# Kernel tuning notes

Hardware: AMD Instinct MI355X
Metric: run time of the kernel (lower is better)

The kernel has to match this reference:

```python
import jax, jax.numpy as jnp
import numpy as np

GRID = 256      # spatial grid (periodic, pseudo-spectral)
BATCH = 8
N_STEPS = 4     # dynamics steps between outputs (layer arg N)
N_OUTPUT = 4    # number of outputs (layer arg n_output)
CH = 32         # Q_network hidden channels
DT = 0.01       # timestep
R_DRAG = 0.05   # linear (Ekman) drag
BETA = 0.5      # beta-plane coefficient
Q_SCALE = 0.01  # Q_callback scaling of network output
IN_W = 1.0      # input_weight
OUT_W = 1.0     # output_weight


def _wavenumbers():
    k = jnp.fft.fftfreq(GRID, 1.0 / GRID).astype(jnp.float32)  # integer wavenumbers
    KX = k[None, :]   # x varies along axis 1
    KY = k[:, None]   # y varies along axis 0
    K2 = KX * KX + KY * KY
    inv_lap = jnp.where(K2 > 0, -1.0 / jnp.where(K2 > 0, K2, 1.0), 0.0)  # psi_hat = -zeta_hat/k^2
    return KX, KY, inv_lap


def _q_network(z, W1, b1, W2, b2):
    # 2-layer 3x3 CNN forcing network on a single [H, W] field.
    x = z[None, :, :, None]  # NHWC
    dn = ('NHWC', 'HWIO', 'NHWC')
    h = jax.lax.conv_general_dilated(x, W1, (1, 1), 'SAME', dimension_numbers=dn) + b1
    h = jax.nn.relu(h)
    q = jax.lax.conv_general_dilated(h, W2, (1, 1), 'SAME', dimension_numbers=dn) + b2
    return q[0, :, :, 0]


def setup_inputs() -> dict:
    key = jax.random.key(0)
    k0, k1, k2, k3 = jax.random.split(key, 4)
    zeta = jax.random.normal(k0, (BATCH, GRID, GRID), dtype=jnp.float32)
    Q_0 = 0.1 * jax.random.normal(k1, (GRID, GRID), dtype=jnp.float32)
    W1 = 0.1 * jax.random.normal(k2, (3, 3, 1, CH), dtype=jnp.float32)
    b1 = jnp.zeros((CH,), dtype=jnp.float32)
    W2 = 0.1 * jax.random.normal(k3, (3, 3, CH, 1), dtype=jnp.float32)
    b2 = jnp.zeros((1,), dtype=jnp.float32)
    return {"zeta": zeta, "Q_0": Q_0, "W1": W1, "b1": b1, "W2": W2, "b2": b2}


def reference(zeta, Q_0, W1, b1, W2, b2):
    KX, KY, inv_lap = _wavenumbers()

    @jax.checkpoint
    def step(_, z):
        # Q_0 + Q_callback(dynamics, Q_network), evaluated before each step
        Q = Q_0 + Q_SCALE * _q_network(z, W1, b1, W2, b2)
        zh = jnp.fft.fft2(z)
        ph = zh * inv_lap                                  # solve nabla^2 psi = zeta
        u = jnp.real(jnp.fft.ifft2(-1j * KY * ph))         # u = -dpsi/dy
        v = jnp.real(jnp.fft.ifft2(1j * KX * ph))          # v =  dpsi/dx
        zx = jnp.real(jnp.fft.ifft2(1j * KX * zh))
        zy = jnp.real(jnp.fft.ifft2(1j * KY * zh))
        adv = u * zx + v * zy
        return z + DT * (-adv - BETA * v - R_DRAG * z + Q)

    def compute_step_outputs(z, _):
        z = jax.lax.fori_loop(0, N_STEPS, step, z)
        return z, z * OUT_W

    def compute_outputs(z0):
        _, outs = jax.lax.scan(compute_step_outputs, z0 * IN_W, None, length=N_OUTPUT)
        return outs  # [n_output, H, W]

    return jax.vmap(compute_outputs)(zeta)  # [batch, n_output, H, W]
```

## Files before the change

kernel.cpp:

```cpp
#include <hip/hip_runtime.h>

#define NG 256
#define PI2F 6.28318530717958647692f
#define PIDX(i) ((i) + ((i) >> 4))

__device__ __forceinline__ float2 f2add(float2 a, float2 b){ return make_float2(a.x+b.x, a.y+b.y); }
__device__ __forceinline__ float2 f2sub(float2 a, float2 b){ return make_float2(a.x-b.x, a.y-b.y); }
__device__ __forceinline__ float2 cmul(float2 a, float2 b){ return make_float2(a.x*b.x - a.y*b.y, a.x*b.y + a.y*b.x); }
__device__ __forceinline__ float comp(float4 v, int p) {
    return p == 0 ? v.x : p == 1 ? v.y : p == 2 ? v.z : v.w;
}
__device__ __forceinline__ float4 f4fma(float4 a, float4 v, float s) {
    return make_float4(fmaf(v.x, s, a.x), fmaf(v.y, s, a.y),
                       fmaf(v.z, s, a.z), fmaf(v.w, s, a.w));
}
__device__ __forceinline__ float dot4(float4 a, float4 b) {
    return a.x * b.x + a.y * b.y + a.z * b.z + a.w * b.w;
}

template<bool INV>
__device__ __forceinline__ void fft256_r4(float2* a, float2* b, const float2* tw,
                                          int u, bool act)
{
#pragma unroll
    for (int st = 0; st < 4; ++st) {
        if (act) {
            const int sl = 2 * st;
            const int q  = u & ((1 << sl) - 1);
            const int j1 = u - q;
            const float2 x0 = a[PIDX(u)];
            const float2 x1 = a[PIDX(u + 64)];
            const float2 x2 = a[PIDX(u + 128)];
            const float2 x3 = a[PIDX(u + 192)];
            float2 w1 = tw[j1];
            if (INV) w1.y = -w1.y;
            const float2 w2 = cmul(w1, w1);
            const float2 w3 = cmul(w1, w2);
            const float2 apc = f2add(x0, x2), amc = f2sub(x0, x2);
            const float2 bpd = f2add(x1, x3), bmd = f2sub(x1, x3);
            const float2 jb  = make_float2(-bmd.y, bmd.x);
            const float2 t0  = f2add(apc, bpd);
            const float2 t2  = f2sub(apc, bpd);
            const float2 t1  = INV ? f2add(amc, jb) : f2sub(amc, jb);
            const float2 t3  = INV ? f2sub(amc, jb) : f2add(amc, jb);
            const int wb = q + (j1 << 2);
            const int ss = 1 << sl;
            b[PIDX(wb)]          = t0;
            b[PIDX(wb + ss)]     = cmul(w1, t1);
            b[PIDX(wb + 2 * ss)] = cmul(w2, t2);
            b[PIDX(wb + 3 * ss)] = cmul(w3, t3);
        }
        __syncthreads();
        float2* tmp = a; a = b; b = tmp;
    }
}

__device__ __forceinline__ void init_tw(float2* tw, int tid)
{
    if (tid < 256) {
        float s, c;
        __sincosf(-PI2F * (float)tid * (1.f / 256.f), &s, &c);
        tw[tid] = make_float2(c, s);
    }
}

#define R_POOL 19456

__global__ void __launch_bounds__(256)
r_kernel(const float* zin, float* zout,
         const float2* __restrict__ Ct0, const float2* __restrict__ Ct1,
         float2* __restrict__ At, const float* __restrict__ Qb,
         float* __restrict__ outp, int do_d, int do_a)
{
    __shared__ __align__(16) char pool[R_POOL];
    float2* tw   = (float2*)pool;
    float2* bufs = (float2*)(pool + 2048);
    const int tid = threadIdx.x;
    const int b   = blockIdx.x & 7;
    const int y0  = (blockIdx.x >> 3) * 2;
    const int j   = tid >> 6, u = tid & 63;

    init_tw(tw, tid);

    if (do_d) {
        float2* A = bufs + j * 272;
        float2* B = bufs + (4 + j) * 272;
        const float2* src = ((j & 1) ? Ct1 : Ct0)
                          + ((size_t)(b * NG + y0 + (j >> 1))) * NG;
#pragma unroll
        for (int r4 = 0; r4 < 4; ++r4) {
            const int x = u + 64 * r4;
            A[PIDX(x)] = src[x];
        }
        __syncthreads();
        fft256_r4<true>(A, B, tw, u, true);

        const float sc = 1.f / 256.f;
        float zn01[2];
#pragma unroll
        for (int r = 0; r < 2; ++r) {
            const float2 uvv = (bufs + (2 * r) * 272)[PIDX(tid)];
            const float2 gzz = (bufs + (2 * r + 1) * 272)[PIDX(tid)];
            const float uu = uvv.x * sc, vv = uvv.y * sc;
            const float zx = gzz.x * sc, zy = gzz.y * sc;
            const int idx = (b * NG + y0 + r) * NG + tid;
            const float z0v = zin[idx];
            const float qv  = Qb[idx];
            const float adv = uu * zx + vv * zy;
            const float zn = z0v + 0.01f * (-adv - 0.5f * vv - 0.05f * z0v + qv);
            zout[idx] = zn;
            if (outp) outp[b * (4 * NG * NG) + (y0 + r) * NG + tid] = zn;
            zn01[r] = zn;
        }
        __syncthreads();
        bufs[PIDX(tid)] = make_float2(zn01[0], zn01[1]);
        __syncthreads();
    } else {
        bufs[PIDX(tid)] = make_float2(zin[(b * NG + y0) * NG + tid],
                                      zin[(b * NG + y0 + 1) * NG + tid]);
        __syncthreads();
    }

    if (do_a) {
        fft256_r4<false>(bufs, bufs + 4 * 272, tw, u, j == 0);
        const int k  = tid;
        const int km = (256 - k) & 255;
        const float2 Zk = bufs[PIDX(k)], Zm = bufs[PIDX(km)];
        const float dx = Zk.x - Zm.x, dy = Zk.y + Zm.y;
        const float4 ov = make_float4(0.5f * (Zk.x + Zm.x), 0.5f * (Zk.y - Zm.y),
                                      0.5f * dy, -0.5f * dx);
        *((float4*)(At + ((size_t)(b * NG + k)) * NG + y0)) = ov;
    }
}

#define COL_POOL 51344

__global__ void __launch_bounds__(512)
col_kernel(const float2* __restrict__ At, float2* __restrict__ Ct0,
           float2* __restrict__ Ct1, const float* __restrict__ zsrc,
           const float* __restrict__ Q0, const float* __restrict__ W1,
           const float* __restrict__ b1, const float* __restrict__ W2,
           const float* __restrict__ b2, float* __restrict__ Qb)
{
    __shared__ __align__(16) char pool[COL_POOL];
    const int tid = threadIdx.x;

    if (blockIdx.x >= 512) {
        float*  zt  = (float*)pool;
        float*  ht  = (float*)(pool + 2240);
        float4* w1s = (float4*)(pool + 48896);
        float4* w2s = (float4*)(pool + 50048);
        float*  b1s = (float*)(pool + 51200);
        float*  b2s = (float*)(pool + 51328);
        const int cb  = blockIdx.x - 512;
        const int b   = cb & 7;
        const int tile = cb >> 3;
        const int ty0 = (tile >> 4) * 16, tx0 = (tile & 15) * 16;

        if (tid < 72) {
            w1s[tid] = ((const float4*)W1)[tid];
            w2s[tid] = ((const float4*)W2)[tid];
        }
        if (tid < 32) b1s[tid] = b1[tid];
        if (tid == 0) b2s[0] = b2[0];

        for (int i = tid; i < 120; i += 512) {
            const int r = i / 6, c4 = i - r * 6;
            const int gy = ty0 - 2 + r;
            const int gx = tx0 - 4 + 4 * c4;
            float4 v = make_float4(0.f, 0.f, 0.f, 0.f);
            if ((unsigned)gy < 256u && (unsigned)gx < 256u)
                v = *((const float4*)&zsrc[(b * NG + gy) * NG + gx]);
            *((float4*)&zt[r * 28 + 4 * c4]) = v;
        }
        __syncthreads();

        if (tid < 360) {
            const int chunk = tid >> 2, cgp = tid & 3;
            const int hy = chunk / 5, hx0 = (chunk - hy * 5) * 4;
            const int k4 = hx0;
            float4 hacc[8];
#pragma unroll
            for (int c = 0; c < 8; ++c) {
                const float bv = b1s[cgp * 8 + c];
                hacc[c] = make_float4(bv, bv, bv, bv);
            }
#pragma unroll
            for (int dy = 0; dy < 3; ++dy) {
                const float* zrow = &zt[(hy + dy) * 28 + k4];
                const float4 Az = *((const float4*)zrow);
                const float4 Bz = *((const float4*)(zrow + 4));
                const float4 W0 = make_float4(Az.z, Az.w, Bz.x, Bz.y);
                const float4 W1v = make_float4(Az.w, Bz.x, Bz.y, Bz.z);
#pragma unroll
                for (int g = 0; g < 2; ++g) {
                    const float4 wa = w1s[(dy * 3 + 0) * 8 + 2 * cgp + g];
                    const float4 wb = w1s[(dy * 3 + 1) * 8 + 2 * cgp + g];
                    const float4 wc = w1s[(dy * 3 + 2) * 8 + 2 * cgp + g];
                    hacc[4*g+0] = f4fma(f4fma(f4fma(hacc[4*g+0], W0, wa.x), W1v, wb.x), Bz, wc.x);
                    hacc[4*g+1] = f4fma(f4fma(f4fma(hacc[4*g+1], W0, wa.y), W1v, wb.y), Bz, wc.y);
                    hacc[4*g+2] = f4fma(f4fma(f4fma(hacc[4*g+2], W0, wa.z), W1v, wb.z), Bz, wc.z);
                    hacc[4*g+3] = f4fma(f4fma(f4fma(hacc[4*g+3], W0, wa.w), W1v, wb.w), Bz, wc.w);
                }
            }
            const int gyh = ty0 - 1 + hy;
            const bool vy = (unsigned)gyh < 256u;
#pragma unroll
            for (int p = 0; p < 4; ++p) {
                const int hxc = hx0 + p;
                if (hxc < 18) {
                    const float mk = (vy && (unsigned)(tx0 - 1 + hxc) < 256u) ? 1.f : 0.f;
                    float* cellp = &ht[(hy * 18 + hxc) * 36];
                    const int s0 = ((2 * cgp + 0 + hxc) & 7) << 2;
                    const int s1 = ((2 * cgp + 1 + hxc) & 7) << 2;
                    const float4 lo = make_float4(
                        mk * fmaxf(comp(hacc[0], p), 0.f), mk * fmaxf(comp(hacc[1], p), 0.f),
                        mk * fmaxf(comp(hacc[2], p), 0.f), mk * fmaxf(comp(hacc[3], p), 0.f));
                    const float4 hi = make_float4(
                        mk * fmaxf(comp(hacc[4], p), 0.f), mk * fmaxf(comp(hacc[5], p), 0.f),
                        mk * fmaxf(comp(hacc[6], p), 0.f), mk * fmaxf(comp(hacc[7], p), 0.f));
                    *((float4*)(cellp + s0)) = lo;
                    *((float4*)(cellp + s1)) = hi;
                }
            }
        }
        __syncthreads();

        {
            const int chunk = tid >> 3, cg = tid & 7;
            const int oy = chunk >> 2, ox4 = (chunk & 3) * 4;
            float q0 = 0.f, q1 = 0.f, q2 = 0.f, q3 = 0.f;
#pragma unroll
            for (int dy = 0; dy < 3; ++dy) {
                const float* hrow = &ht[((oy + dy) * 18 + ox4) * 36];
                const float4 wA = w2s[(dy * 3 + 0) * 8 + cg];
                const float4 wB = w2s[(dy * 3 + 1) * 8 + cg];
                const float4 wC = w2s[(dy * 3 + 2) * 8 + cg];
#pragma unroll
                for (int jj = 0; jj < 6; ++jj) {
                    const float4 hv = *((const float4*)(hrow + jj * 36
                                        + (((cg + ox4 + jj) & 7) << 2)));
                    if (jj <= 3) {
                        const float d = dot4(hv, wA);
                        if (jj == 0) q0 += d; else if (jj == 1) q1 += d;
                        else if (jj == 2) q2 += d; else q3 += d;
                    }
                    if (jj >= 1 && jj <= 4) {
                        const float d = dot4(hv, wB);
                        if (jj == 1) q0 += d; else if (jj == 2) q1 += d;
                        else if (jj == 3) q2 += d; else q3 += d;
                    }
                    if (jj >= 2) {
                        const float d = dot4(hv, wC);
                        if (jj == 2) q0 += d; else if (jj == 3) q1 += d;
                        else if (jj == 4) q2 += d; else q3 += d;
                    }
                }
            }
#pragma unroll
            for (int s = 1; s < 8; s <<= 1) {
                q0 += __shfl_xor(q0, s); q1 += __shfl_xor(q1, s);
                q2 += __shfl_xor(q2, s); q3 += __shfl_xor(q3, s);
            }
            if (cg == 0) {
                const int gy = ty0 + oy, gx = tx0 + ox4;
                const float4 Qv = *((const float4*)&Q0[gy * NG + gx]);
                const float bb = b2s[0];
                const float4 o = make_float4(
                    Qv.x + 0.01f * (q0 + bb), Qv.y + 0.01f * (q1 + bb),
                    Qv.z + 0.01f * (q2 + bb), Qv.w + 0.01f * (q3 + bb));
                *((float4*)&Qb[(b * NG + gy) * NG + gx]) = o;
            }
        }
    } else {
        float2* tw   = (float2*)pool;
        float2* bufs = (float2*)(pool + 2048);
        const int bid = blockIdx.x;
        const int b  = bid & 7;
        const int kg = bid >> 3;
        const int j8 = tid >> 6, u = tid & 63;

        init_tw(tw, tid);
        if (j8 < 4) {
            const int kxl = 4 * kg + j8;
            float2* A = bufs + j8 * 272;
            const float2* src = At + ((size_t)(b * NG + kxl)) * NG;
#pragma unroll
            for (int r = 0; r < 4; ++r) {
                const int x = u + 64 * r;
                A[PIDX(x)] = src[x];
            }
        }
        __syncthreads();
        fft256_r4<false>(bufs + j8 * 272, bufs + (4 + (j8 & 3)) * 272, tw, u, j8 < 4);

        if (tid < 256) {
            const int jl = tid >> 6;
            const int kxl = 4 * kg + jl;
            float2* A = bufs + jl * 272;
            float2* C = bufs + (8 + jl) * 272;
            const float kxv = (kxl < 128) ? (float)kxl : (float)(kxl - 256);
            const float kxm = (kxl == 128) ? 0.f : kxv;
#pragma unroll
            for (int r = 0; r < 4; ++r) {
                const int ky = u + 64 * r;
                const float kyv = (ky < 128) ? (float)ky : (float)(ky - 256);
                const float kym = (ky == 128) ? 0.f : kyv;
                const float K2 = kxv * kxv + kyv * kyv;
                const float il = (K2 > 0.f) ? (-1.f / K2) : 0.f;
                const float2 Z = A[PIDX(ky)];
                const float ar = -kxm * il, ai = -kym * il;
                A[PIDX(ky)] = make_float2(ar * Z.x - ai * Z.y, ar * Z.y + ai * Z.x);
                C[PIDX(ky)] = make_float2(-kym * Z.x - kxm * Z.y, -kym * Z.y + kxm * Z.x);
            }
        }
        __syncthreads();

        float2* ia = (j8 < 4) ? bufs + j8 * 272 : bufs + (8 + (j8 - 4)) * 272;
        float2* ib = (j8 < 4) ? bufs + (4 + j8) * 272 : bufs + (12 + (j8 - 4)) * 272;
        fft256_r4<true>(ia, ib, tw, u, true);

        const float sc = 1.f / 256.f;
        const int y = tid & 255;
        float2 ov[4];
        if (tid < 256) {
#pragma unroll
            for (int jj = 0; jj < 4; ++jj) {
                const float2 r0 = (bufs + jj * 272)[PIDX(y)];
                ov[jj] = make_float2(r0.x * sc, r0.y * sc);
            }
            float4* dst = (float4*)(Ct0 + ((size_t)(b * NG + y)) * NG + 4 * kg);
            dst[0] = ((float4*)ov)[0];
            dst[1] = ((float4*)ov)[1];
        } else {
#pragma unroll
            for (int jj = 0; jj < 4; ++jj) {
                const float2 r1 = (bufs + (8 + jj) * 272)[PIDX(y)];
                ov[jj] = make_float2(r1.x * sc, r1.y * sc);
            }
            float4* dst = (float4*)(Ct1 + ((size_t)(b * NG + y)) * NG + 4 * kg);
            dst[0] = ((float4*)ov)[0];
            dst[1] = ((float4*)ov)[1];
        }
    }
}

extern "C" void kernel_launch(void* const* d_in, const int* in_sizes, int n_in,
                              void* d_out, int out_size, void* d_ws, size_t ws_size,
                              hipStream_t stream)
{
    const float* zeta = (const float*)d_in[0];
    const float* Q0   = (const float*)d_in[1];
    const float* W1   = (const float*)d_in[2];
    const float* b1   = (const float*)d_in[3];
    const float* W2   = (const float*)d_in[4];
    const float* b2   = (const float*)d_in[5];
    float* outp = (float*)d_out;

    char* ws = (char*)d_ws;
    float*  zws = (float*)(ws);
    float*  Qb  = (float*)(ws + (2u << 20));
    float2* At  = (float2*)(ws + (4u << 20));
    float2* Ct0 = (float2*)(ws + (8u << 20));
    float2* Ct1 = (float2*)(ws + (12u << 20));
    if (ws_size < (16u << 20)) return;

    r_kernel<<<1024, 256, 0, stream>>>(zeta, zws, Ct0, Ct1, At, Qb,
                                       nullptr, 0, 1);
    for (int j = 1; j <= 16; ++j) {
        const float* zp = (j == 1) ? zeta : zws;
        col_kernel<<<2560, 512, 0, stream>>>(At, Ct0, Ct1, zp,
                                             Q0, W1, b1, W2, b2, Qb);
        float* op = (j % 4 == 0) ? (outp + (size_t)(j / 4 - 1) * NG * NG)
                                 : nullptr;
        r_kernel<<<1024, 256, 0, stream>>>(zp, zws, Ct0, Ct1, At, Qb,
                                           op, 1, (j < 16) ? 1 : 0);
    }
}
```

Measured before the change: 551.9 us.

## Double per-block work in row FFT and CNN kernels to halve block counts

The row kernel now processes four rows per 512-thread block instead of two per 256-thread block, running two independent inverse and forward FFT groups. The CNN part of the column kernel now covers a 16x32 tile per block by looping over two 16x16 subtiles and sharing one halo load and one weight load. The aim is fewer blocks and less repeated twiddle, weight and halo setup. The cost is more shared memory per block, extra barriers inside the CNN loop, and a serialized two-pass CNN that may reduce latency hiding.

```diff
diff --git a/kernel.cpp b/kernel.cpp
--- a/kernel.cpp
+++ b/kernel.cpp
@@ -64,9 +64,9 @@
     }
 }
 
-#define R_POOL 19456
-
-__global__ void __launch_bounds__(256)
+#define R_POOL 36864
+
+__global__ void __launch_bounds__(512)
 r_kernel(const float* zin, float* zout,
          const float2* __restrict__ Ct0, const float2* __restrict__ Ct1,
          float2* __restrict__ At, const float* __restrict__ Qb,
@@ -77,14 +77,15 @@
     float2* bufs = (float2*)(pool + 2048);
     const int tid = threadIdx.x;
     const int b   = blockIdx.x & 7;
-    const int y0  = (blockIdx.x >> 3) * 2;
+    const int y0  = (blockIdx.x >> 3) * 4;
     const int j   = tid >> 6, u = tid & 63;
+    const int col = tid & 255, rp = tid >> 8;
 
     init_tw(tw, tid);
 
     if (do_d) {
         float2* A = bufs + j * 272;
-        float2* B = bufs + (4 + j) * 272;
+        float2* B = bufs + (8 + j) * 272;
         const float2* src = ((j & 1) ? Ct1 : Ct0)
                           + ((size_t)(b * NG + y0 + (j >> 1))) * NG;
 #pragma unroll
@@ -99,41 +100,46 @@
         float zn01[2];
 #pragma unroll
         for (int r = 0; r < 2; ++r) {
-            const float2 uvv = (bufs + (2 * r) * 272)[PIDX(tid)];
-            const float2 gzz = (bufs + (2 * r + 1) * 272)[PIDX(tid)];
+            const int rr = 2 * rp + r;
+            const float2 uvv = (bufs + (2 * rr) * 272)[PIDX(col)];
+            const float2 gzz = (bufs + (2 * rr + 1) * 272)[PIDX(col)];
             const float uu = uvv.x * sc, vv = uvv.y * sc;
             const float zx = gzz.x * sc, zy = gzz.y * sc;
-            const int idx = (b * NG + y0 + r) * NG + tid;
+            const int idx = (b * NG + y0 + rr) * NG + col;
             const float z0v = zin[idx];
             const float qv  = Qb[idx];
             const float adv = uu * zx + vv * zy;
             const float zn = z0v + 0.01f * (-adv - 0.5f * vv - 0.05f * z0v + qv);
             zout[idx] = zn;
-            if (outp) outp[b * (4 * NG * NG) + (y0 + r) * NG + tid] = zn;
+            if (outp) outp[b * (4 * NG * NG) + (y0 + rr) * NG + col] = zn;
             zn01[r] = zn;
         }
         __syncthreads();
-        bufs[PIDX(tid)] = make_float2(zn01[0], zn01[1]);
+        (bufs + 2 * rp * 272)[PIDX(col)] = make_float2(zn01[0], zn01[1]);
         __syncthreads();
     } else {
-        bufs[PIDX(tid)] = make_float2(zin[(b * NG + y0) * NG + tid],
-                                      zin[(b * NG + y0 + 1) * NG + tid]);
+        (bufs + 2 * rp * 272)[PIDX(col)] =
+            make_float2(zin[(b * NG + y0 + 2 * rp) * NG + col],
+                        zin[(b * NG + y0 + 2 * rp + 1) * NG + col]);
         __syncthreads();
     }
 
     if (do_a) {
-        fft256_r4<false>(bufs, bufs + 4 * 272, tw, u, j == 0);
-        const int k  = tid;
+        const int jj = (j < 2) ? j : 1;
+        fft256_r4<false>(bufs + 2 * jj * 272, bufs + (8 + 2 * jj) * 272,
+                         tw, u, j < 2);
+        const int k  = col;
         const int km = (256 - k) & 255;
-        const float2 Zk = bufs[PIDX(k)], Zm = bufs[PIDX(km)];
+        const float2* Aj = bufs + 2 * rp * 272;
+        const float2 Zk = Aj[PIDX(k)], Zm = Aj[PIDX(km)];
         const float dx = Zk.x - Zm.x, dy = Zk.y + Zm.y;
         const float4 ov = make_float4(0.5f * (Zk.x + Zm.x), 0.5f * (Zk.y - Zm.y),
                                       0.5f * dy, -0.5f * dx);
-        *((float4*)(At + ((size_t)(b * NG + k)) * NG + y0)) = ov;
-    }
-}
-
-#define COL_POOL 51344
+        *((float4*)(At + ((size_t)(b * NG + k)) * NG + y0 + 2 * rp)) = ov;
+    }
+}
+
+#define COL_POOL 52624
 
 __global__ void __launch_bounds__(512)
 col_kernel(const float2* __restrict__ At, float2* __restrict__ Ct0,
@@ -147,15 +153,16 @@
 
     if (blockIdx.x >= 512) {
         float*  zt  = (float*)pool;
-        float*  ht  = (float*)(pool + 2240);
-        float4* w1s = (float4*)(pool + 48896);
-        float4* w2s = (float4*)(pool + 50048);
-        float*  b1s = (float*)(pool + 51200);
-        float*  b2s = (float*)(pool + 51328);
+        float*  ht  = (float*)(pool + 3520);
+        float4* w1s = (float4*)(pool + 50176);
+        float4* w2s = (float4*)(pool + 51328);
+        float*  b1s = (float*)(pool + 52480);
+        float*  b2s = (float*)(pool + 52608);
         const int cb  = blockIdx.x - 512;
         const int b   = cb & 7;
-        const int tile = cb >> 3;
-        const int ty0 = (tile >> 4) * 16, tx0 = (tile & 15) * 16;
+        const int pr  = cb >> 3;
+        const int ty0 = (pr >> 3) * 16;
+        const int tx0 = (pr & 7) * 32;
 
         if (tid < 72) {
             w1s[tid] = ((const float4*)W1)[tid];
@@ -164,113 +171,117 @@
         if (tid < 32) b1s[tid] = b1[tid];
         if (tid == 0) b2s[0] = b2[0];
 
-        for (int i = tid; i < 120; i += 512) {
-            const int r = i / 6, c4 = i - r * 6;
+        for (int i = tid; i < 200; i += 512) {
+            const int r = i / 10, c4 = i - r * 10;
             const int gy = ty0 - 2 + r;
             const int gx = tx0 - 4 + 4 * c4;
             float4 v = make_float4(0.f, 0.f, 0.f, 0.f);
             if ((unsigned)gy < 256u && (unsigned)gx < 256u)
                 v = *((const float4*)&zsrc[(b * NG + gy) * NG + gx]);
-            *((float4*)&zt[r * 28 + 4 * c4]) = v;
-        }
-        __syncthreads();
-
-        if (tid < 360) {
-            const int chunk = tid >> 2, cgp = tid & 3;
-            const int hy = chunk / 5, hx0 = (chunk - hy * 5) * 4;
-            const int k4 = hx0;
-            float4 hacc[8];
-#pragma unroll
-            for (int c = 0; c < 8; ++c) {
-                const float bv = b1s[cgp * 8 + c];
-                hacc[c] = make_float4(bv, bv, bv, bv);
-            }
-#pragma unroll
-            for (int dy = 0; dy < 3; ++dy) {
-                const float* zrow = &zt[(hy + dy) * 28 + k4];
-                const float4 Az = *((const float4*)zrow);
-                const float4 Bz = *((const float4*)(zrow + 4));
-                const float4 W0 = make_float4(Az.z, Az.w, Bz.x, Bz.y);
-                const float4 W1v = make_float4(Az.w, Bz.x, Bz.y, Bz.z);
-#pragma unroll
-                for (int g = 0; g < 2; ++g) {
-                    const float4 wa = w1s[(dy * 3 + 0) * 8 + 2 * cgp + g];
-                    const float4 wb = w1s[(dy * 3 + 1) * 8 + 2 * cgp + g];
-                    const float4 wc = w1s[(dy * 3 + 2) * 8 + 2 * cgp + g];
-                    hacc[4*g+0] = f4fma(f4fma(f4fma(hacc[4*g+0], W0, wa.x), W1v, wb.x), Bz, wc.x);
-                    hacc[4*g+1] = f4fma(f4fma(f4fma(hacc[4*g+1], W0, wa.y), W1v, wb.y), Bz, wc.y);
-                    hacc[4*g+2] = f4fma(f4fma(f4fma(hacc[4*g+2], W0, wa.z), W1v, wb.z), Bz, wc.z);
-                    hacc[4*g+3] = f4fma(f4fma(f4fma(hacc[4*g+3], W0, wa.w), W1v, wb.w), Bz, wc.w);
-                }
-            }
-            const int gyh = ty0 - 1 + hy;
-            const bool vy = (unsigned)gyh < 256u;
-#pragma unroll
-            for (int p = 0; p < 4; ++p) {
-                const int hxc = hx0 + p;
-                if (hxc < 18) {
-                    const float mk = (vy && (unsigned)(tx0 - 1 + hxc) < 256u) ? 1.f : 0.f;
-                    float* cellp = &ht[(hy * 18 + hxc) * 36];
-                    const int s0 = ((2 * cgp + 0 + hxc) & 7) << 2;
-                    const int s1 = ((2 * cgp + 1 + hxc) & 7) << 2;
-                    const float4 lo = make_float4(
-                        mk * fmaxf(comp(hacc[0], p), 0.f), mk * fmaxf(comp(hacc[1], p), 0.f),
-                        mk * fmaxf(comp(hacc[2], p), 0.f), mk * fmaxf(comp(hacc[3], p), 0.f));
-                    const float4 hi = make_float4(
-                        mk * fmaxf(comp(hacc[4], p), 0.f), mk * fmaxf(comp(hacc[5], p), 0.f),
-                        mk * fmaxf(comp(hacc[6], p), 0.f), mk * fmaxf(comp(hacc[7], p), 0.f));
-                    *((float4*)(cellp + s0)) = lo;
-                    *((float4*)(cellp + s1)) = hi;
-                }
-            }
-        }
-        __syncthreads();
-
-        {
-            const int chunk = tid >> 3, cg = tid & 7;
-            const int oy = chunk >> 2, ox4 = (chunk & 3) * 4;
-            float q0 = 0.f, q1 = 0.f, q2 = 0.f, q3 = 0.f;
-#pragma unroll
-            for (int dy = 0; dy < 3; ++dy) {
-                const float* hrow = &ht[((oy + dy) * 18 + ox4) * 36];
-                const float4 wA = w2s[(dy * 3 + 0) * 8 + cg];
-                const float4 wB = w2s[(dy * 3 + 1) * 8 + cg];
-                const float4 wC = w2s[(dy * 3 + 2) * 8 + cg];
-#pragma unroll
-                for (int jj = 0; jj < 6; ++jj) {
-                    const float4 hv = *((const float4*)(hrow + jj * 36
-                                        + (((cg + ox4 + jj) & 7) << 2)));
-                    if (jj <= 3) {
-                        const float d = dot4(hv, wA);
-                        if (jj == 0) q0 += d; else if (jj == 1) q1 += d;
-                        else if (jj == 2) q2 += d; else q3 += d;
+            *((float4*)&zt[r * 44 + 4 * c4]) = v;
+        }
+        __syncthreads();
+
+        for (int t = 0; t < 2; ++t) {
+            const int txt = tx0 + 16 * t;
+            if (tid < 360) {
+                const int chunk = tid >> 2, cgp = tid & 3;
+                const int hy = chunk / 5, hx0 = (chunk - hy * 5) * 4;
+                const int k4 = 16 * t + hx0;
+                float4 hacc[8];
+#pragma unroll
+                for (int c = 0; c < 8; ++c) {
+                    const float bv = b1s[cgp * 8 + c];
+                    hacc[c] = make_float4(bv, bv, bv, bv);
+                }
+#pragma unroll
+                for (int dy = 0; dy < 3; ++dy) {
+                    const float* zrow = &zt[(hy + dy) * 44 + k4];
+                    const float4 Az = *((const float4*)zrow);
+                    const float4 Bz = *((const float4*)(zrow + 4));
+                    const float4 W0 = make_float4(Az.z, Az.w, Bz.x, Bz.y);
+                    const float4 W1v = make_float4(Az.w, Bz.x, Bz.y, Bz.z);
+#pragma unroll
+                    for (int g = 0; g < 2; ++g) {
+                        const float4 wa = w1s[(dy * 3 + 0) * 8 + 2 * cgp + g];
+                        const float4 wb = w1s[(dy * 3 + 1) * 8 + 2 * cgp + g];
+                        const float4 wc = w1s[(dy * 3 + 2) * 8 + 2 * cgp + g];
+                        hacc[4*g+0] = f4fma(f4fma(f4fma(hacc[4*g+0], W0, wa.x), W1v, wb.x), Bz, wc.x);
+                        hacc[4*g+1] = f4fma(f4fma(f4fma(hacc[4*g+1], W0, wa.y), W1v, wb.y), Bz, wc.y);
+                        hacc[4*g+2] = f4fma(f4fma(f4fma(hacc[4*g+2], W0, wa.z), W1v, wb.z), Bz, wc.z);
+                        hacc[4*g+3] = f4fma(f4fma(f4fma(hacc[4*g+3], W0, wa.w), W1v, wb.w), Bz, wc.w);
                     }
-                    if (jj >= 1 && jj <= 4) {
-                        const float d = dot4(hv, wB);
-                        if (jj == 1) q0 += d; else if (jj == 2) q1 += d;
-                        else if (jj == 3) q2 += d; else q3 += d;
+                }
+                const int gyh = ty0 - 1 + hy;
+                const bool vy = (unsigned)gyh < 256u;
+#pragma unroll
+                for (int p = 0; p < 4; ++p) {
+                    const int hxc = hx0 + p;
+                    if (hxc < 18) {
+                        const float mk = (vy && (unsigned)(txt - 1 + hxc) < 256u) ? 1.f : 0.f;
+                        float* cellp = &ht[(hy * 18 + hxc) * 36];
+                        const int s0 = ((2 * cgp + 0 + hxc) & 7) << 2;
+                        const int s1 = ((2 * cgp + 1 + hxc) & 7) << 2;
+                        const float4 lo = make_float4(
+                            mk * fmaxf(comp(hacc[0], p), 0.f), mk * fmaxf(comp(hacc[1], p), 0.f),
+                            mk * fmaxf(comp(hacc[2], p), 0.f), mk * fmaxf(comp(hacc[3], p), 0.f));
+                        const float4 hi = make_float4(
+                            mk * fmaxf(comp(hacc[4], p), 0.f), mk * fmaxf(comp(hacc[5], p), 0.f),
+                            mk * fmaxf(comp(hacc[6], p), 0.f), mk * fmaxf(comp(hacc[7], p), 0.f));
+                        *((float4*)(cellp + s0)) = lo;
+                        *((float4*)(cellp + s1)) = hi;
                     }
-                    if (jj >= 2) {
-                        const float d = dot4(hv, wC);
-                        if (jj == 2) q0 += d; else if (jj == 3) q1 += d;
-                        else if (jj == 4) q2 += d; else q3 += d;
+                }
+            }
+            __syncthreads();
+
+            {
+                const int chunk = tid >> 3, cg = tid & 7;
+                const int oy = chunk >> 2, ox4 = (chunk & 3) * 4;
+                float q0 = 0.f, q1 = 0.f, q2 = 0.f, q3 = 0.f;
+#pragma unroll
+                for (int dy = 0; dy < 3; ++dy) {
+                    const float* hrow = &ht[((oy + dy) * 18 + ox4) * 36];
+                    const float4 wA = w2s[(dy * 3 + 0) * 8 + cg];
+                    const float4 wB = w2s[(dy * 3 + 1) * 8 + cg];
+                    const float4 wC = w2s[(dy * 3 + 2) * 8 + cg];
+#pragma unroll
+                    for (int jj = 0; jj < 6; ++jj) {
+                        const float4 hv = *((const float4*)(hrow + jj * 36
+                                            + (((cg + ox4 + jj) & 7) << 2)));
+                        if (jj <= 3) {
+                            const float d = dot4(hv, wA);
+                            if (jj == 0) q0 += d; else if (jj == 1) q1 += d;
+                            else if (jj == 2) q2 += d; else q3 += d;
+                        }
+                        if (jj >= 1 && jj <= 4) {
+                            const float d = dot4(hv, wB);
+                            if (jj == 1) q0 += d; else if (jj == 2) q1 += d;
+                            else if (jj == 3) q2 += d; else q3 += d;
+                        }
+                        if (jj >= 2) {
+                            const float d = dot4(hv, wC);
+                            if (jj == 2) q0 += d; else if (jj == 3) q1 += d;
+                            else if (jj == 4) q2 += d; else q3 += d;
+                        }
                     }
                 }
-            }
-#pragma unroll
-            for (int s = 1; s < 8; s <<= 1) {
-                q0 += __shfl_xor(q0, s); q1 += __shfl_xor(q1, s);
-                q2 += __shfl_xor(q2, s); q3 += __shfl_xor(q3, s);
-            }
-            if (cg == 0) {
-                const int gy = ty0 + oy, gx = tx0 + ox4;
-                const float4 Qv = *((const float4*)&Q0[gy * NG + gx]);
-                const float bb = b2s[0];
-                const float4 o = make_float4(
-                    Qv.x + 0.01f * (q0 + bb), Qv.y + 0.01f * (q1 + bb),
-                    Qv.z + 0.01f * (q2 + bb), Qv.w + 0.01f * (q3 + bb));
-                *((float4*)&Qb[(b * NG + gy) * NG + gx]) = o;
-            }
+#pragma unroll
+                for (int s = 1; s < 8; s <<= 1) {
+                    q0 += __shfl_xor(q0, s); q1 += __shfl_xor(q1, s);
+                    q2 += __shfl_xor(q2, s); q3 += __shfl_xor(q3, s);
+                }
+                if (cg == 0) {
+                    const int gy = ty0 + oy, gx = txt + ox4;
+                    const float4 Qv = *((const float4*)&Q0[gy * NG + gx]);
+                    const float bb = b2s[0];
+                    const float4 o = make_float4(
+                        Qv.x + 0.01f * (q0 + bb), Qv.y + 0.01f * (q1 + bb),
+                        Qv.z + 0.01f * (q2 + bb), Qv.w + 0.01f * (q3 + bb));
+                    *((float4*)&Qb[(b * NG + gy) * NG + gx]) = o;
+                }
+            }
+            __syncthreads();
         }
     } else {
         float2* tw   = (float2*)pool;
@@ -365,15 +376,15 @@
     float2* Ct1 = (float2*)(ws + (12u << 20));
     if (ws_size < (16u << 20)) return;
 
-    r_kernel<<<1024, 256, 0, stream>>>(zeta, zws, Ct0, Ct1, At, Qb,
-                                       nullptr, 0, 1);
+    r_kernel<<<512, 512, 0, stream>>>(zeta, zws, Ct0, Ct1, At, Qb,
+                                      nullptr, 0, 1);
     for (int j = 1; j <= 16; ++j) {
         const float* zp = (j == 1) ? zeta : zws;
-        col_kernel<<<2560, 512, 0, stream>>>(At, Ct0, Ct1, zp,
+        col_kernel<<<1536, 512, 0, stream>>>(At, Ct0, Ct1, zp,
                                              Q0, W1, b1, W2, b2, Qb);
         float* op = (j % 4 == 0) ? (outp + (size_t)(j / 4 - 1) * NG * NG)
                                  : nullptr;
-        r_kernel<<<1024, 256, 0, stream>>>(zp, zws, Ct0, Ct1, At, Qb,
-                                           op, 1, (j < 16) ? 1 : 0);
-    }
-}
+        r_kernel<<<512, 512, 0, stream>>>(zp, zws, Ct0, Ct1, At, Qb,
+                                          op, 1, (j < 16) ? 1 : 0);
+    }
+}
```

New measurement: 694.3 us. 1.26x slower.
